# Kernel optimization log

Measured on AMD Instinct MI355X. Metric: run time of the kernel, lower is better.

## Reference

```python
import jax, jax.numpy as jnp
import numpy as np

N_ROW = 50000
N_COL = 50000
E = 1_200_000
D_IN = 64
D_H = 128


def _gconv(h_src, src, dst, w_e, W, b, n_src, n_dst):
    """DGL GraphConv(norm='both') with edge weights: symmetric degree norm
    (unweighted degrees, clamped to >=1), u_mul_e message, sum reduce, then linear."""
    ones = jnp.ones_like(w_e)
    out_deg = jnp.clip(jax.ops.segment_sum(ones, src, num_segments=n_src), 1.0)
    in_deg = jnp.clip(jax.ops.segment_sum(ones, dst, num_segments=n_dst), 1.0)
    hs = h_src * jax.lax.rsqrt(out_deg)[:, None]          # [n_src, F] pre-norm
    m = hs[src] * w_e[:, None]                            # [E, F] gather + edge weight
    agg = jax.ops.segment_sum(m, dst, num_segments=n_dst)  # [n_dst, F] scatter-sum
    agg = agg * jax.lax.rsqrt(in_deg)[:, None]
    return agg @ W + b


def setup_inputs() -> dict:
    key = jax.random.key(0)
    ks = jax.random.split(key, 16)
    return {
        'feat_row': jax.random.normal(ks[0], (N_ROW, D_IN), jnp.float32),
        'feat_col': jax.random.normal(ks[1], (N_COL, D_IN), jnp.float32),
        'src_rc': jax.random.randint(ks[2], (E,), 0, N_ROW),
        'dst_rc': jax.random.randint(ks[3], (E,), 0, N_COL),
        'w_rc': jax.random.uniform(ks[4], (E,), jnp.float32),
        'src_cr': jax.random.randint(ks[5], (E,), 0, N_COL),
        'dst_cr': jax.random.randint(ks[6], (E,), 0, N_ROW),
        'w_cr': jax.random.uniform(ks[7], (E,), jnp.float32),
        'W0_rc': jax.random.normal(ks[8], (D_IN, D_H), jnp.float32) / np.float32(np.sqrt(D_IN)),
        'b0_rc': jnp.zeros((D_H,), jnp.float32),
        'W0_cr': jax.random.normal(ks[9], (D_IN, D_H), jnp.float32) / np.float32(np.sqrt(D_IN)),
        'b0_cr': jnp.zeros((D_H,), jnp.float32),
        'W1_rc': jax.random.normal(ks[10], (D_H, D_H), jnp.float32) / np.float32(np.sqrt(D_H)),
        'b1_rc': jnp.zeros((D_H,), jnp.float32),
        'W1_cr': jax.random.normal(ks[11], (D_H, D_H), jnp.float32) / np.float32(np.sqrt(D_H)),
        'b1_cr': jnp.zeros((D_H,), jnp.float32),
    }


def reference(feat_row, feat_col, src_rc, dst_rc, w_rc, src_cr, dst_cr, w_cr,
              W0_rc, b0_rc, W0_cr, b0_cr, W1_rc, b1_rc, W1_cr, b1_cr):
    # Layer 1 (HeteroGraphConv, sum across relations; each dst type has one relation) + ReLU
    h_col1 = jax.nn.relu(_gconv(feat_row, src_rc, dst_rc, w_rc, W0_rc, b0_rc, N_ROW, N_COL))
    h_row1 = jax.nn.relu(_gconv(feat_col, src_cr, dst_cr, w_cr, W0_cr, b0_cr, N_COL, N_ROW))
    # Layer 2 + ReLU
    h_col2 = jax.nn.relu(_gconv(h_row1, src_rc, dst_rc, w_rc, W1_rc, b1_rc, N_ROW, N_COL))
    h_row2 = jax.nn.relu(_gconv(h_col1, src_cr, dst_cr, w_cr, W1_cr, b1_cr, N_COL, N_ROW))
    # dgl.mean_nodes per ntype (single graph -> [1, D_H]), summed over ntypes
    hg = jnp.mean(h_row2, axis=0, keepdims=True) + jnp.mean(h_col2, axis=0, keepdims=True)
    return hg
```

## Files before the change

kernel.cpp:

```cpp
#include <hip/hip_runtime.h>
#include <stdint.h>

constexpr int NROW = 50000;
constexpr int NCOL = 50000;
constexpr int DH   = 128;
constexpr int NTAB = 200000;
constexpr int HB   = 12500;
constexpr int HBLK = 64;
constexpr int DGRID = 1250;
constexpr int GGRID = 2048;
constexpr int CH    = 500;

typedef __attribute__((ext_vector_type(8))) short short8;
typedef __attribute__((ext_vector_type(4))) float f32x4;
typedef __attribute__((ext_vector_type(2))) float f32x2;

__device__ __forceinline__ float bf_hi(unsigned u) { return __uint_as_float(u & 0xffff0000u); }
__device__ __forceinline__ unsigned short f2bf(float f) {
    unsigned u = __float_as_uint(f);
    return (unsigned short)((u + 0x7fffu + ((u >> 16) & 1u)) >> 16);
}

__device__ __forceinline__ unsigned char f2fp8(float f) {
    unsigned b = __float_as_uint(f);
    unsigned s = (b >> 24) & 0x80u;
    unsigned mag = b & 0x7fffffffu;
    if (mag >= 0x43e00000u) return (unsigned char)(s | 0x7eu);
    unsigned r = mag + 0x7ffffu + ((mag >> 20) & 1u);
    int e = (int)(r >> 23) - 120;
    if (e < 1) {
        float af = __uint_as_float(mag);
        unsigned m = (unsigned)(af * 512.f + 0.5f);
        if (m > 8u) m = 8u;
        return (unsigned char)(s | m);
    }
    return (unsigned char)(s | (unsigned)(e << 3) | ((r >> 20) & 7u));
}

#if defined(__has_builtin) && __has_builtin(__builtin_amdgcn_cvt_pk_f32_fp8)
__device__ __forceinline__ f32x2 fp8x2f(unsigned v) {
    return __builtin_amdgcn_cvt_pk_f32_fp8((int)v, false);
}
__device__ __forceinline__ f32x4 fp8x4f(unsigned v) {
    f32x2 lo = __builtin_amdgcn_cvt_pk_f32_fp8((int)v, false);
    f32x2 hi = __builtin_amdgcn_cvt_pk_f32_fp8((int)v, true);
    f32x4 r; r.x = lo.x; r.y = lo.y; r.z = hi.x; r.w = hi.y; return r;
}
#else
__device__ __forceinline__ float fp8_1(unsigned u) {
    unsigned s = (u & 0x80u) << 24, em = u & 0x7fu;
    if (em >= 8u) return __uint_as_float(s | ((em + 960u) << 20));
    float v = (float)em * 0.001953125f;
    return (u & 0x80u) ? -v : v;
}
__device__ __forceinline__ f32x2 fp8x2f(unsigned v) {
    f32x2 r; r.x = fp8_1(v & 0xffu); r.y = fp8_1((v >> 8) & 0xffu); return r;
}
__device__ __forceinline__ f32x4 fp8x4f(unsigned v) {
    f32x4 r; r.x = fp8_1(v & 0xffu); r.y = fp8_1((v >> 8) & 0xffu);
    r.z = fp8_1((v >> 16) & 0xffu); r.w = fp8_1((v >> 24) & 0xffu); return r;
}
#endif

__global__ __launch_bounds__(512) void hist_lds(
        const int* __restrict__ s_rc, const int* __restrict__ d_rc,
        const int* __restrict__ s_cr, const int* __restrict__ d_cr,
        unsigned short* __restrict__ partial, int E) {
    __shared__ int h[HB];
    const int sec = blockIdx.x >> 6;
    const int blk = blockIdx.x & (HBLK - 1);
    const int tab = sec >> 2;
    const int lo  = (sec & 3) * HB;
    const int* __restrict__ arr = (tab == 0) ? s_rc : (tab == 1) ? d_rc
                                 : (tab == 2) ? s_cr : d_cr;
    for (int i = threadIdx.x; i < HB; i += blockDim.x) h[i] = 0;
    __syncthreads();
    const int stride = HBLK * blockDim.x;
    for (int i = blk * blockDim.x + threadIdx.x; i < E; i += stride) {
        int id = arr[i] - lo;
        if ((unsigned)id < (unsigned)HB) atomicAdd(&h[id], 1);
    }
    __syncthreads();
    unsigned short* __restrict__ out = partial + ((size_t)sec * HBLK + blk) * HB;
    for (int i = threadIdx.x; i < HB; i += blockDim.x) out[i] = (unsigned short)h[i];
}

__global__ void reduce_norms2(const unsigned short* __restrict__ partial, int* __restrict__ cnt,
                              float* __restrict__ norms) {
    int stride = gridDim.x * blockDim.x;
    for (int i = blockIdx.x * blockDim.x + threadIdx.x; i < NTAB; i += stride) {
        int t = i / 50000;
        int r = i - t * 50000;
        int q = r / HB;
        int j = r - q * HB;
        const unsigned short* __restrict__ p = partial + ((size_t)(t * 4 + q) * HBLK) * HB + j;
        int s = 0;
#pragma unroll
        for (int b = 0; b < HBLK; ++b) s += p[(size_t)b * HB];
        cnt[i] = s;
        norms[i] = 1.0f / sqrtf((float)max(s, 1));
    }
}

__global__ __launch_bounds__(256) void scanA(const int* __restrict__ cnt, int* __restrict__ bsum) {
    __shared__ int red[256];
    const int c = blockIdx.x;
    const int* __restrict__ cbl = cnt + ((c >= 100) ? 150000 : 50000);
    const int j0 = (c % 100) * CH;
    int s = 0;
    for (int i = threadIdx.x; i < CH; i += 256) s += cbl[j0 + i];
    red[threadIdx.x] = s;
    __syncthreads();
    for (int off = 128; off > 0; off >>= 1) {
        if (threadIdx.x < off) red[threadIdx.x] += red[threadIdx.x + off];
        __syncthreads();
    }
    if (threadIdx.x == 0) bsum[c] = red[0];
}

__global__ void scanB(const int* __restrict__ bsum, int* __restrict__ cbase) {
    __shared__ int b[200];
    for (int i = threadIdx.x; i < 200; i += blockDim.x) b[i] = bsum[i];
    __syncthreads();
    if (threadIdx.x < 2) {
        int run = 0;
        const int o = threadIdx.x * 100;
        for (int k = 0; k < 100; ++k) { cbase[o + k] = run; run += b[o + k]; }
    }
}

__global__ __launch_bounds__(512) void scanC(const int* __restrict__ cnt,
                                             const int* __restrict__ cbase,
                                             int* __restrict__ ptr_rc, int* __restrict__ ptr_cr,
                                             int E) {
    __shared__ int buf[512];
    const int c = blockIdx.x;
    const int table = (c >= 100);
    const int* __restrict__ cbl = cnt + (table ? 150000 : 50000);
    int* __restrict__ ptr = table ? ptr_cr : ptr_rc;
    const int j0 = (c % 100) * CH;
    const int t = threadIdx.x;
    const int v = (t < CH) ? cbl[j0 + t] : 0;
    buf[t] = v;
    __syncthreads();
    for (int off = 1; off < 512; off <<= 1) {
        int tmp = (t >= off) ? buf[t - off] : 0;
        __syncthreads();
        buf[t] += tmp;
        __syncthreads();
    }
    if (t < CH) ptr[j0 + t] = cbase[c] + buf[t] - v;
    if ((c % 100) == 99 && t == 0) ptr[50000] = E;
}

__global__ void block_starts(const unsigned short* __restrict__ partial, int* __restrict__ bstart,
                             const int* __restrict__ ptr_rc, const int* __restrict__ ptr_cr) {
    int stride = gridDim.x * blockDim.x;
    for (int i = blockIdx.x * blockDim.x + threadIdx.x; i < 8 * HB; i += stride) {
        int fsec = i / HB;
        int j = i - fsec * HB;
        int rel = fsec >> 2, q = fsec & 3;
        int histsec = rel * 8 + 4 + q;
        const int* __restrict__ ptr = rel ? ptr_cr : ptr_rc;
        int run = ptr[q * HB + j];
        const unsigned short* __restrict__ p = partial + ((size_t)histsec * HBLK) * HB + j;
        int* __restrict__ o = bstart + ((size_t)fsec * HBLK) * HB + j;
#pragma unroll
        for (int b = 0; b < HBLK; ++b) {
            o[(size_t)b * HB] = run;
            run += p[(size_t)b * HB];
        }
    }
}

__global__ __launch_bounds__(512) void csr_fill_sorted(
        const int* __restrict__ sA, const int* __restrict__ dA,
        const float* __restrict__ wA, const float* __restrict__ routA, unsigned* __restrict__ pairA,
        const int* __restrict__ sB, const int* __restrict__ dB,
        const float* __restrict__ wB, const float* __restrict__ routB, unsigned* __restrict__ pairB,
        const int* __restrict__ bstart, int E) {
    __shared__ int offs[HB];
    const int fsec = blockIdx.x & 7;
    const int blk  = blockIdx.x >> 3;
    const int rel = fsec >> 2, q = fsec & 3;
    const int lo = q * HB;
    const int* __restrict__ src  = rel ? sB : sA;
    const int* __restrict__ dst  = rel ? dB : dA;
    const float* __restrict__ w  = rel ? wB : wA;
    const float* __restrict__ ro = rel ? routB : routA;
    unsigned* __restrict__ pair  = rel ? pairB : pairA;
    const int* __restrict__ bs = bstart + ((size_t)fsec * HBLK + blk) * HB;
    for (int i = threadIdx.x; i < HB; i += blockDim.x) offs[i] = bs[i];
    __syncthreads();
    const int stride = HBLK * blockDim.x;
    for (int i = blk * blockDim.x + threadIdx.x; i < E; i += stride) {
        int id = dst[i] - lo;
        if ((unsigned)id < (unsigned)HB) {
            int pos = atomicAdd(&offs[id], 1);
            int s = src[i];
            pair[pos] = (unsigned)s | ((unsigned)f2bf(w[i] * ro[s]) << 16);
        }
    }
}

__global__ void prep_tables(const float4* __restrict__ fr, const float4* __restrict__ fc,
                            unsigned* __restrict__ f8r, unsigned* __restrict__ f8c, int nq,
                            const float* __restrict__ W0a, const float* __restrict__ W0b,
                            const float* __restrict__ W1a, const float* __restrict__ W1b,
                            unsigned short* __restrict__ wt) {
    const int total = 2 * nq + 49152;
    int stride = gridDim.x * blockDim.x;
    for (int i = blockIdx.x * blockDim.x + threadIdx.x; i < total; i += stride) {
        if (i < 2 * nq) {
            bool second = i >= nq;
            int k = second ? i - nq : i;
            float4 v = second ? fc[k] : fr[k];
            unsigned o = (unsigned)f2fp8(v.x) | ((unsigned)f2fp8(v.y) << 8)
                       | ((unsigned)f2fp8(v.z) << 16) | ((unsigned)f2fp8(v.w) << 24);
            if (second) f8c[k] = o; else f8r[k] = o;
        } else {
            int j = i - 2 * nq;
            const float* W; int K, base;
            if (j < 8192)       { W = W0a; K = 64;  base = 0; }
            else if (j < 16384) { W = W0b; K = 64;  base = 8192;  j -= 8192; }
            else if (j < 32768) { W = W1a; K = 128; base = 16384; j -= 16384; }
            else                { W = W1b; K = 128; base = 32768; j -= 32768; }
            int n = j / K, k = j - n * K;
            wt[base + n * K + k] = f2bf(W[k * DH + n]);
        }
    }
}

__global__ void gather64_2(const uint8_t* __restrict__ hA, const int* __restrict__ ptrA,
                           const unsigned* __restrict__ pairA, unsigned short* __restrict__ aggA,
                           const uint8_t* __restrict__ hB, const int* __restrict__ ptrB,
                           const unsigned* __restrict__ pairB, unsigned short* __restrict__ aggB,
                           int n) {
    const int low  = blockIdx.x & 7;
    const int rel  = low >> 2;
    const int bid  = (blockIdx.x >> 3) * 4 + (low & 3);
    const uint8_t* __restrict__ h = rel ? hB : hA;
    const int* __restrict__ ptr  = rel ? ptrB : ptrA;
    const unsigned* __restrict__ pair = rel ? pairB : pairA;
    unsigned short* __restrict__ agg  = rel ? aggB : aggA;
    const int gw   = (bid * blockDim.x + threadIdx.x) >> 6;
    const int nw   = (GGRID * blockDim.x) >> 6;
    const int lane = threadIdx.x & 63;
    const int qtr  = lane >> 4;
    const unsigned coff = (unsigned)((lane & 15) << 2);
    for (int node = gw; node < n; node += nw) {
        const int beg = ptr[node], end = ptr[node + 1];
        float a0[2] = {0.f, 0.f}, a1[2] = {0.f, 0.f}, a2[2] = {0.f, 0.f}, a3[2] = {0.f, 0.f};
        int j = beg + qtr;
        for (; j + 4 < end; j += 8) {
            unsigned p0 = pair[j], p1 = pair[j + 4];
            unsigned hv0 = *reinterpret_cast<const unsigned*>(&h[((p0 & 0xffffu) << 6) + coff]);
            unsigned hv1 = *reinterpret_cast<const unsigned*>(&h[((p1 & 0xffffu) << 6) + coff]);
            f32x4 d0 = fp8x4f(hv0), d1 = fp8x4f(hv1);
            float w0 = bf_hi(p0), w1 = bf_hi(p1);
            a0[0] = fmaf(d0.x, w0, a0[0]); a1[0] = fmaf(d0.y, w0, a1[0]);
            a2[0] = fmaf(d0.z, w0, a2[0]); a3[0] = fmaf(d0.w, w0, a3[0]);
            a0[1] = fmaf(d1.x, w1, a0[1]); a1[1] = fmaf(d1.y, w1, a1[1]);
            a2[1] = fmaf(d1.z, w1, a2[1]); a3[1] = fmaf(d1.w, w1, a3[1]);
        }
        for (; j < end; j += 4) {
            unsigned p = pair[j];
            unsigned hv = *reinterpret_cast<const unsigned*>(&h[((p & 0xffffu) << 6) + coff]);
            f32x4 d = fp8x4f(hv);
            float w = bf_hi(p);
            a0[0] = fmaf(d.x, w, a0[0]); a1[0] = fmaf(d.y, w, a1[0]);
            a2[0] = fmaf(d.z, w, a2[0]); a3[0] = fmaf(d.w, w, a3[0]);
        }
        float s0 = a0[0] + a0[1], s1 = a1[0] + a1[1];
        float s2 = a2[0] + a2[1], s3 = a3[0] + a3[1];
        s0 += __shfl_xor(s0, 16); s0 += __shfl_xor(s0, 32);
        s1 += __shfl_xor(s1, 16); s1 += __shfl_xor(s1, 32);
        s2 += __shfl_xor(s2, 16); s2 += __shfl_xor(s2, 32);
        s3 += __shfl_xor(s3, 16); s3 += __shfl_xor(s3, 32);
        if (lane < 16) {
            uint2 pk;
            pk.x = (unsigned)f2bf(s0) | ((unsigned)f2bf(s1) << 16);
            pk.y = (unsigned)f2bf(s2) | ((unsigned)f2bf(s3) << 16);
            *reinterpret_cast<uint2*>(&agg[(size_t)node * 64 + ((lane & 15) << 2)]) = pk;
        }
    }
}

__global__ __launch_bounds__(256) void dense64_2(
        const unsigned short* __restrict__ aggA, const float* __restrict__ rinA,
        const unsigned short* __restrict__ wtA, const float* __restrict__ bA,
        unsigned short* __restrict__ outA,
        const unsigned short* __restrict__ aggB, const float* __restrict__ rinB,
        const unsigned short* __restrict__ wtB, const float* __restrict__ bB,
        unsigned short* __restrict__ outB, int n) {
    constexpr int K = 64, NCH = 2;
    const int rel = blockIdx.x >= DGRID;
    const int bid = rel ? blockIdx.x - DGRID : blockIdx.x;
    const unsigned short* __restrict__ agg = rel ? aggB : aggA;
    const float* __restrict__ rin = rel ? rinB : rinA;
    const unsigned short* __restrict__ wt = rel ? wtB : wtA;
    const float* __restrict__ b = rel ? bB : bA;
    unsigned short* __restrict__ outbf = rel ? outB : outA;

    const int wave = threadIdx.x >> 6;
    const int lane = threadIdx.x & 63;
    const int lrow = lane & 15;
    const int kgrp = lane >> 4;
    const int c0   = wave * 32;

    short8 bfr[2][NCH];
#pragma unroll
    for (int t = 0; t < 2; ++t)
#pragma unroll
        for (int ch = 0; ch < NCH; ++ch)
            bfr[t][ch] = *reinterpret_cast<const short8*>(
                &wt[(size_t)(c0 + t * 16 + lrow) * K + ch * 32 + kgrp * 8]);

    const float bias0 = b[c0 + lrow], bias1 = b[c0 + 16 + lrow];
    const int nstrip = n >> 4;
    for (int s = bid; s < nstrip; s += DGRID) {
        const int r0 = s << 4;
        f32x4 d0 = {0.f, 0.f, 0.f, 0.f}, d1 = {0.f, 0.f, 0.f, 0.f};
#pragma unroll
        for (int ch = 0; ch < NCH; ++ch) {
            short8 af = *reinterpret_cast<const short8*>(
                &agg[(size_t)(r0 + lrow) * K + ch * 32 + kgrp * 8]);
            d0 = __builtin_amdgcn_mfma_f32_16x16x32_bf16(af, bfr[0][ch], d0, 0, 0, 0);
            d1 = __builtin_amdgcn_mfma_f32_16x16x32_bf16(af, bfr[1][ch], d1, 0, 0, 0);
        }
#pragma unroll
        for (int i = 0; i < 4; ++i) {
            const int row = r0 + kgrp * 4 + i;
            const float rv = rin[row];
            outbf[(size_t)row * DH + c0 + lrow]      = f2bf(fmaxf(fmaf(rv, d0[i], bias0), 0.f));
            outbf[(size_t)row * DH + c0 + 16 + lrow] = f2bf(fmaxf(fmaf(rv, d1[i], bias1), 0.f));
        }
    }
}

__global__ __launch_bounds__(256) void h1t_gemm2(
        const unsigned short* __restrict__ hA, const unsigned short* __restrict__ wtA,
        uint8_t* __restrict__ htA,
        const unsigned short* __restrict__ hB, const unsigned short* __restrict__ wtB,
        uint8_t* __restrict__ htB, int n) {
    constexpr int K = 128, NCH = 4;
    const int rel = blockIdx.x >= DGRID;
    const int bid = rel ? blockIdx.x - DGRID : blockIdx.x;
    const unsigned short* __restrict__ h = rel ? hB : hA;
    const unsigned short* __restrict__ wt = rel ? wtB : wtA;
    uint8_t* __restrict__ ht = rel ? htB : htA;

    const int wave = threadIdx.x >> 6;
    const int lane = threadIdx.x & 63;
    const int lrow = lane & 15;
    const int kgrp = lane >> 4;
    const int c0   = wave * 32;

    short8 bfr[2][NCH];
#pragma unroll
    for (int t = 0; t < 2; ++t)
#pragma unroll
        for (int ch = 0; ch < NCH; ++ch)
            bfr[t][ch] = *reinterpret_cast<const short8*>(
                &wt[(size_t)(c0 + t * 16 + lrow) * K + ch * 32 + kgrp * 8]);

    const int nstrip = n >> 4;
    for (int s = bid; s < nstrip; s += DGRID) {
        const int r0 = s << 4;
        f32x4 d0 = {0.f, 0.f, 0.f, 0.f}, d1 = {0.f, 0.f, 0.f, 0.f};
#pragma unroll
        for (int ch = 0; ch < NCH; ++ch) {
            short8 af = *reinterpret_cast<const short8*>(
                &h[(size_t)(r0 + lrow) * K + ch * 32 + kgrp * 8]);
            d0 = __builtin_amdgcn_mfma_f32_16x16x32_bf16(af, bfr[0][ch], d0, 0, 0, 0);
            d1 = __builtin_amdgcn_mfma_f32_16x16x32_bf16(af, bfr[1][ch], d1, 0, 0, 0);
        }
#pragma unroll
        for (int i = 0; i < 4; ++i) {
            const int row = r0 + kgrp * 4 + i;
            ht[(size_t)row * DH + c0 + lrow]      = f2fp8(d0[i]);
            ht[(size_t)row * DH + c0 + 16 + lrow] = f2fp8(d1[i]);
        }
    }
}

__global__ __launch_bounds__(256) void gather_final(
        const uint8_t* __restrict__ htA, const int* __restrict__ ptrA,
        const unsigned* __restrict__ pairA, const float* __restrict__ rinA,
        const float* __restrict__ bA,
        const uint8_t* __restrict__ htB, const int* __restrict__ ptrB,
        const unsigned* __restrict__ pairB, const float* __restrict__ rinB,
        const float* __restrict__ bB,
        float* __restrict__ partsum, int n, float invn) {
    const int low  = blockIdx.x & 7;
    const int rel  = low >> 2;
    const int chf  = (low >> 1) & 1;
    const int bid  = (blockIdx.x >> 3) * 2 + (low & 1);
    const uint8_t* __restrict__ ht = rel ? htB : htA;
    const int* __restrict__ ptr  = rel ? ptrB : ptrA;
    const unsigned* __restrict__ pair = rel ? pairB : pairA;
    const float* __restrict__ rin = rel ? rinB : rinA;
    const float* __restrict__ b   = rel ? bB : bA;

    const int gw   = (bid * blockDim.x + threadIdx.x) >> 6;
    const int nw   = ((GGRID / 2) * blockDim.x) >> 6;
    const int lane = threadIdx.x & 63;
    const int h2   = lane >> 5;
    const unsigned coff = (unsigned)(chf * 64 + ((lane & 31) << 1));
    const float b0v = b[coff], b1v = b[coff + 1];
    float m0 = 0.f, m1 = 0.f;

    for (int node = gw; node < n; node += nw) {
        const int beg = ptr[node], end = ptr[node + 1];
        float a0[4] = {0.f, 0.f, 0.f, 0.f}, a1[4] = {0.f, 0.f, 0.f, 0.f};
        int j = beg + h2;
        for (; j + 6 < end; j += 8) {
            unsigned p[4], hv[4];
#pragma unroll
            for (int u = 0; u < 4; ++u) p[u] = pair[j + 2 * u];
#pragma unroll
            for (int u = 0; u < 4; ++u)
                hv[u] = *reinterpret_cast<const unsigned short*>(&ht[((p[u] & 0xffffu) << 7) + coff]);
#pragma unroll
            for (int u = 0; u < 4; ++u) {
                f32x2 d = fp8x2f(hv[u]);
                float w = bf_hi(p[u]);
                a0[u] = fmaf(d.x, w, a0[u]);
                a1[u] = fmaf(d.y, w, a1[u]);
            }
        }
        for (; j < end; j += 2) {
            unsigned p = pair[j];
            unsigned hv = *reinterpret_cast<const unsigned short*>(&ht[((p & 0xffffu) << 7) + coff]);
            f32x2 d = fp8x2f(hv);
            float w = bf_hi(p);
            a0[0] = fmaf(d.x, w, a0[0]);
            a1[0] = fmaf(d.y, w, a1[0]);
        }
        float sx = (a0[0] + a0[1]) + (a0[2] + a0[3]);
        float sy = (a1[0] + a1[1]) + (a1[2] + a1[3]);
        sx += __shfl_xor(sx, 32);
        sy += __shfl_xor(sy, 32);
        const float rv = rin[node];
        m0 += fmaxf(fmaf(rv, sx, b0v), 0.f);
        m1 += fmaxf(fmaf(rv, sy, b1v), 0.f);
    }

    __shared__ float red[4][64];
    const int wv = threadIdx.x >> 6;
    if (h2 == 0) {
        red[wv][(lane & 31) * 2]     = m0;
        red[wv][(lane & 31) * 2 + 1] = m1;
    }
    __syncthreads();
    if (threadIdx.x < 64) {
        float s = red[0][threadIdx.x] + red[1][threadIdx.x]
                + red[2][threadIdx.x] + red[3][threadIdx.x];
        partsum[(size_t)blockIdx.x * 64 + threadIdx.x] = s * invn;
    }
}

__global__ void reduce_out2(const float* __restrict__ partsum, float* __restrict__ out, int nblk) {
    const int t = threadIdx.x;
    const int ch = t >> 6, c = t & 63;
    float s = 0.f;
    for (int b = blockIdx.x; b < nblk; b += gridDim.x)
        if (((b >> 1) & 1) == ch) s += partsum[(size_t)b * 64 + c];
    atomicAdd(&out[t], s);
}

extern "C" void kernel_launch(void* const* d_in, const int* in_sizes, int n_in,
                              void* d_out, int out_size, void* d_ws, size_t ws_size,
                              hipStream_t stream) {
    const float* feat_row = (const float*)d_in[0];
    const float* feat_col = (const float*)d_in[1];
    const int*   src_rc   = (const int*)d_in[2];
    const int*   dst_rc   = (const int*)d_in[3];
    const float* w_rc     = (const float*)d_in[4];
    const int*   src_cr   = (const int*)d_in[5];
    const int*   dst_cr   = (const int*)d_in[6];
    const float* w_cr     = (const float*)d_in[7];
    const float* W0_rc    = (const float*)d_in[8];
    const float* b0_rc    = (const float*)d_in[9];
    const float* W0_cr    = (const float*)d_in[10];
    const float* b0_cr    = (const float*)d_in[11];
    const float* W1_rc    = (const float*)d_in[12];
    const float* b1_rc    = (const float*)d_in[13];
    const float* W1_cr    = (const float*)d_in[14];
    const float* b1_cr    = (const float*)d_in[15];
    const int E = in_sizes[2];
    float* out = (float*)d_out;

    int*   cnt     = (int*)d_ws;
    float* norms   = (float*)(cnt + 200000);
    int*   ptr_rc  = (int*)(norms + 200000);
    int*   ptr_cr  = ptr_rc + 50004;
    int*   bsum    = ptr_cr + 50004;
    int*   cbase   = bsum + 200;
    unsigned* pair_rc = (unsigned*)(cbase + 216);
    unsigned* pair_cr = pair_rc + E;
    unsigned short* agg_col = (unsigned short*)(pair_cr + E);
    unsigned short* agg_row = agg_col + (size_t)NCOL * 64;
    uint8_t* f8_row = (uint8_t*)(agg_row + (size_t)NROW * 64);
    uint8_t* f8_col = f8_row + (size_t)NROW * 64;
    unsigned short* h_col1 = (unsigned short*)(f8_col + (size_t)NCOL * 64);
    unsigned short* h_row1 = h_col1 + (size_t)NCOL * DH;
    uint8_t* ht_row = (uint8_t*)(h_row1 + (size_t)NROW * DH);
    uint8_t* ht_col = ht_row + (size_t)NROW * DH;
    float* partsum = (float*)(ht_col + (size_t)NCOL * DH);
    unsigned short* wt = (unsigned short*)(partsum + (size_t)2 * GGRID * DH);
    unsigned short* partial = (unsigned short*)agg_col;
    int* bstart = (int*)(partial + (size_t)16 * HBLK * HB);

    float* r_out_rc = norms;
    float* r_in_rc  = norms + NROW;
    float* r_out_cr = norms + NROW + NCOL;
    float* r_in_cr  = norms + NROW + 2 * NCOL;

    unsigned short* wt0_rc = wt;
    unsigned short* wt0_cr = wt + 8192;
    unsigned short* wt1_rc = wt + 16384;
    unsigned short* wt1_cr = wt + 32768;

    hist_lds<<<16 * HBLK, 512, 0, stream>>>(src_rc, dst_rc, src_cr, dst_cr, partial, E);
    reduce_norms2<<<512, 256, 0, stream>>>(partial, cnt, norms);
    scanA<<<200, 256, 0, stream>>>(cnt, bsum);
    scanB<<<1, 256, 0, stream>>>(bsum, cbase);
    scanC<<<200, 512, 0, stream>>>(cnt, cbase, ptr_rc, ptr_cr, E);
    block_starts<<<400, 256, 0, stream>>>(partial, bstart, ptr_rc, ptr_cr);
    csr_fill_sorted<<<8 * HBLK, 512, 0, stream>>>(
        src_rc, dst_rc, w_rc, r_out_rc, pair_rc,
        src_cr, dst_cr, w_cr, r_out_cr, pair_cr, bstart, E);

    prep_tables<<<2048, 256, 0, stream>>>((const float4*)feat_row, (const float4*)feat_col,
                                          (unsigned*)f8_row, (unsigned*)f8_col, NROW * 64 / 4,
                                          W0_rc, W0_cr, W1_rc, W1_cr, wt);

    gather64_2<<<2 * GGRID, 256, 0, stream>>>(f8_row, ptr_rc, pair_rc, agg_col,
                                              f8_col, ptr_cr, pair_cr, agg_row, NCOL);
    dense64_2<<<2 * DGRID, 256, 0, stream>>>(agg_col, r_in_rc, wt0_rc, b0_rc, h_col1,
                                             agg_row, r_in_cr, wt0_cr, b0_cr, h_row1, NCOL);

    h1t_gemm2<<<2 * DGRID, 256, 0, stream>>>(h_row1, wt1_rc, ht_row,
                                             h_col1, wt1_cr, ht_col, NROW);
    hipMemsetAsync(out, 0, DH * sizeof(float), stream);
    gather_final<<<2 * GGRID, 256, 0, stream>>>(
        ht_row, ptr_rc, pair_rc, r_in_rc, b1_rc,
        ht_col, ptr_cr, pair_cr, r_in_cr, b1_cr,
        partsum, NCOL, 1.0f / NCOL);
    reduce_out2<<<64, 128, 0, stream>>>(partsum, out, 2 * GGRID);
}
```

Baseline: 347.0 us.

## Split fp8 layer-2 table into two 64-column halves and widen gather64 unroll

The fp8 output of the layer-2 transform is stored as two separate 64-byte-per-row tables, one per column half, instead of a single 128-byte-row table. Each gather_final pass then touches a compact table with a denser row stride, which is meant to improve cache locality. Separately, gather64_2 now uses half-waves with 2 columns per lane and 8 independent edge loads in flight instead of quarter-waves with 4 columns. This raises memory-level parallelism at the cost of narrower per-lane loads and more registers.

```diff
diff --git a/kernel.cpp b/kernel.cpp
--- a/kernel.cpp
+++ b/kernel.cpp
@@ -41,11 +41,6 @@
 __device__ __forceinline__ f32x2 fp8x2f(unsigned v) {
     return __builtin_amdgcn_cvt_pk_f32_fp8((int)v, false);
 }
-__device__ __forceinline__ f32x4 fp8x4f(unsigned v) {
-    f32x2 lo = __builtin_amdgcn_cvt_pk_f32_fp8((int)v, false);
-    f32x2 hi = __builtin_amdgcn_cvt_pk_f32_fp8((int)v, true);
-    f32x4 r; r.x = lo.x; r.y = lo.y; r.z = hi.x; r.w = hi.y; return r;
-}
 #else
 __device__ __forceinline__ float fp8_1(unsigned u) {
     unsigned s = (u & 0x80u) << 24, em = u & 0x7fu;
@@ -55,10 +50,6 @@
 }
 __device__ __forceinline__ f32x2 fp8x2f(unsigned v) {
     f32x2 r; r.x = fp8_1(v & 0xffu); r.y = fp8_1((v >> 8) & 0xffu); return r;
-}
-__device__ __forceinline__ f32x4 fp8x4f(unsigned v) {
-    f32x4 r; r.x = fp8_1(v & 0xffu); r.y = fp8_1((v >> 8) & 0xffu);
-    r.z = fp8_1((v >> 16) & 0xffu); r.w = fp8_1((v >> 24) & 0xffu); return r;
 }
 #endif
 
@@ -246,42 +237,42 @@
     const int gw   = (bid * blockDim.x + threadIdx.x) >> 6;
     const int nw   = (GGRID * blockDim.x) >> 6;
     const int lane = threadIdx.x & 63;
-    const int qtr  = lane >> 4;
-    const unsigned coff = (unsigned)((lane & 15) << 2);
+    const int half = lane >> 5;
+    const int c    = (lane & 31) << 1;
     for (int node = gw; node < n; node += nw) {
         const int beg = ptr[node], end = ptr[node + 1];
-        float a0[2] = {0.f, 0.f}, a1[2] = {0.f, 0.f}, a2[2] = {0.f, 0.f}, a3[2] = {0.f, 0.f};
-        int j = beg + qtr;
-        for (; j + 4 < end; j += 8) {
-            unsigned p0 = pair[j], p1 = pair[j + 4];
-            unsigned hv0 = *reinterpret_cast<const unsigned*>(&h[((p0 & 0xffffu) << 6) + coff]);
-            unsigned hv1 = *reinterpret_cast<const unsigned*>(&h[((p1 & 0xffffu) << 6) + coff]);
-            f32x4 d0 = fp8x4f(hv0), d1 = fp8x4f(hv1);
-            float w0 = bf_hi(p0), w1 = bf_hi(p1);
-            a0[0] = fmaf(d0.x, w0, a0[0]); a1[0] = fmaf(d0.y, w0, a1[0]);
-            a2[0] = fmaf(d0.z, w0, a2[0]); a3[0] = fmaf(d0.w, w0, a3[0]);
-            a0[1] = fmaf(d1.x, w1, a0[1]); a1[1] = fmaf(d1.y, w1, a1[1]);
-            a2[1] = fmaf(d1.z, w1, a2[1]); a3[1] = fmaf(d1.w, w1, a3[1]);
-        }
-        for (; j < end; j += 4) {
+        float ax[8], ay[8];
+#pragma unroll
+        for (int u = 0; u < 8; ++u) { ax[u] = 0.f; ay[u] = 0.f; }
+        int j = beg + half;
+        for (; j + 14 < end; j += 16) {
+            unsigned p[8], hv[8];
+#pragma unroll
+            for (int u = 0; u < 8; ++u) p[u] = pair[j + 2 * u];
+#pragma unroll
+            for (int u = 0; u < 8; ++u)
+                hv[u] = *reinterpret_cast<const unsigned short*>(&h[((p[u] & 0xffffu) << 6) + c]);
+#pragma unroll
+            for (int u = 0; u < 8; ++u) {
+                f32x2 d = fp8x2f(hv[u]);
+                float w = bf_hi(p[u]);
+                ax[u] = fmaf(d.x, w, ax[u]); ay[u] = fmaf(d.y, w, ay[u]);
+            }
+        }
+        for (; j < end; j += 2) {
             unsigned p = pair[j];
-            unsigned hv = *reinterpret_cast<const unsigned*>(&h[((p & 0xffffu) << 6) + coff]);
-            f32x4 d = fp8x4f(hv);
+            unsigned hv = *reinterpret_cast<const unsigned short*>(&h[((p & 0xffffu) << 6) + c]);
+            f32x2 d = fp8x2f(hv);
             float w = bf_hi(p);
-            a0[0] = fmaf(d.x, w, a0[0]); a1[0] = fmaf(d.y, w, a1[0]);
-            a2[0] = fmaf(d.z, w, a2[0]); a3[0] = fmaf(d.w, w, a3[0]);
-        }
-        float s0 = a0[0] + a0[1], s1 = a1[0] + a1[1];
-        float s2 = a2[0] + a2[1], s3 = a3[0] + a3[1];
-        s0 += __shfl_xor(s0, 16); s0 += __shfl_xor(s0, 32);
-        s1 += __shfl_xor(s1, 16); s1 += __shfl_xor(s1, 32);
-        s2 += __shfl_xor(s2, 16); s2 += __shfl_xor(s2, 32);
-        s3 += __shfl_xor(s3, 16); s3 += __shfl_xor(s3, 32);
-        if (lane < 16) {
-            uint2 pk;
-            pk.x = (unsigned)f2bf(s0) | ((unsigned)f2bf(s1) << 16);
-            pk.y = (unsigned)f2bf(s2) | ((unsigned)f2bf(s3) << 16);
-            *reinterpret_cast<uint2*>(&agg[(size_t)node * 64 + ((lane & 15) << 2)]) = pk;
+            ax[0] = fmaf(d.x, w, ax[0]); ay[0] = fmaf(d.y, w, ay[0]);
+        }
+        float ax_ = ((ax[0] + ax[1]) + (ax[2] + ax[3])) + ((ax[4] + ax[5]) + (ax[6] + ax[7]));
+        float ay_ = ((ay[0] + ay[1]) + (ay[2] + ay[3])) + ((ay[4] + ay[5]) + (ay[6] + ay[7]));
+        ax_ += __shfl_xor(ax_, 32);
+        ay_ += __shfl_xor(ay_, 32);
+        if (half == 0) {
+            unsigned pk = (unsigned)f2bf(ax_) | ((unsigned)f2bf(ay_) << 16);
+            *reinterpret_cast<unsigned*>(&agg[(size_t)node * 64 + c]) = pk;
         }
     }
 }
@@ -340,21 +331,22 @@
 
 __global__ __launch_bounds__(256) void h1t_gemm2(
         const unsigned short* __restrict__ hA, const unsigned short* __restrict__ wtA,
-        uint8_t* __restrict__ htA,
+        uint8_t* __restrict__ htA0, uint8_t* __restrict__ htA1,
         const unsigned short* __restrict__ hB, const unsigned short* __restrict__ wtB,
-        uint8_t* __restrict__ htB, int n) {
+        uint8_t* __restrict__ htB0, uint8_t* __restrict__ htB1, int n) {
     constexpr int K = 128, NCH = 4;
     const int rel = blockIdx.x >= DGRID;
     const int bid = rel ? blockIdx.x - DGRID : blockIdx.x;
     const unsigned short* __restrict__ h = rel ? hB : hA;
     const unsigned short* __restrict__ wt = rel ? wtB : wtA;
-    uint8_t* __restrict__ ht = rel ? htB : htA;
 
     const int wave = threadIdx.x >> 6;
     const int lane = threadIdx.x & 63;
     const int lrow = lane & 15;
     const int kgrp = lane >> 4;
     const int c0   = wave * 32;
+    uint8_t* __restrict__ ht = (wave < 2) ? (rel ? htB0 : htA0) : (rel ? htB1 : htA1);
+    const int cb = c0 & 63;
 
     short8 bfr[2][NCH];
 #pragma unroll
@@ -378,25 +370,25 @@
 #pragma unroll
         for (int i = 0; i < 4; ++i) {
             const int row = r0 + kgrp * 4 + i;
-            ht[(size_t)row * DH + c0 + lrow]      = f2fp8(d0[i]);
-            ht[(size_t)row * DH + c0 + 16 + lrow] = f2fp8(d1[i]);
+            ht[((size_t)row << 6) + cb + lrow]      = f2fp8(d0[i]);
+            ht[((size_t)row << 6) + cb + 16 + lrow] = f2fp8(d1[i]);
         }
     }
 }
 
 __global__ __launch_bounds__(256) void gather_final(
-        const uint8_t* __restrict__ htA, const int* __restrict__ ptrA,
-        const unsigned* __restrict__ pairA, const float* __restrict__ rinA,
-        const float* __restrict__ bA,
-        const uint8_t* __restrict__ htB, const int* __restrict__ ptrB,
-        const unsigned* __restrict__ pairB, const float* __restrict__ rinB,
-        const float* __restrict__ bB,
+        const uint8_t* __restrict__ htA0, const uint8_t* __restrict__ htA1,
+        const int* __restrict__ ptrA, const unsigned* __restrict__ pairA,
+        const float* __restrict__ rinA, const float* __restrict__ bA,
+        const uint8_t* __restrict__ htB0, const uint8_t* __restrict__ htB1,
+        const int* __restrict__ ptrB, const unsigned* __restrict__ pairB,
+        const float* __restrict__ rinB, const float* __restrict__ bB,
         float* __restrict__ partsum, int n, float invn) {
     const int low  = blockIdx.x & 7;
     const int rel  = low >> 2;
     const int chf  = (low >> 1) & 1;
     const int bid  = (blockIdx.x >> 3) * 2 + (low & 1);
-    const uint8_t* __restrict__ ht = rel ? htB : htA;
+    const uint8_t* __restrict__ ht = rel ? (chf ? htB1 : htB0) : (chf ? htA1 : htA0);
     const int* __restrict__ ptr  = rel ? ptrB : ptrA;
     const unsigned* __restrict__ pair = rel ? pairB : pairA;
     const float* __restrict__ rin = rel ? rinB : rinA;
@@ -406,8 +398,8 @@
     const int nw   = ((GGRID / 2) * blockDim.x) >> 6;
     const int lane = threadIdx.x & 63;
     const int h2   = lane >> 5;
-    const unsigned coff = (unsigned)(chf * 64 + ((lane & 31) << 1));
-    const float b0v = b[coff], b1v = b[coff + 1];
+    const unsigned coff = (unsigned)((lane & 31) << 1);
+    const float b0v = b[chf * 64 + coff], b1v = b[chf * 64 + coff + 1];
     float m0 = 0.f, m1 = 0.f;
 
     for (int node = gw; node < n; node += nw) {
@@ -420,7 +412,7 @@
             for (int u = 0; u < 4; ++u) p[u] = pair[j + 2 * u];
 #pragma unroll
             for (int u = 0; u < 4; ++u)
-                hv[u] = *reinterpret_cast<const unsigned short*>(&ht[((p[u] & 0xffffu) << 7) + coff]);
+                hv[u] = *reinterpret_cast<const unsigned short*>(&ht[((p[u] & 0xffffu) << 6) + coff]);
 #pragma unroll
             for (int u = 0; u < 4; ++u) {
                 f32x2 d = fp8x2f(hv[u]);
@@ -431,7 +423,7 @@
         }
         for (; j < end; j += 2) {
             unsigned p = pair[j];
-            unsigned hv = *reinterpret_cast<const unsigned short*>(&ht[((p & 0xffffu) << 7) + coff]);
+            unsigned hv = *reinterpret_cast<const unsigned short*>(&ht[((p & 0xffffu) << 6) + coff]);
             f32x2 d = fp8x2f(hv);
             float w = bf_hi(p);
             a0[0] = fmaf(d.x, w, a0[0]);
@@ -505,10 +497,12 @@
     uint8_t* f8_col = f8_row + (size_t)NROW * 64;
     unsigned short* h_col1 = (unsigned short*)(f8_col + (size_t)NCOL * 64);
     unsigned short* h_row1 = h_col1 + (size_t)NCOL * DH;
-    uint8_t* ht_row = (uint8_t*)(h_row1 + (size_t)NROW * DH);
-    uint8_t* ht_col = ht_row + (size_t)NROW * DH;
-    float* partsum = (float*)(ht_col + (size_t)NCOL * DH);
-    unsigned short* wt = (unsigned short*)(partsum + (size_t)2 * GGRID * DH);
+    uint8_t* ht_row0 = (uint8_t*)(h_row1 + (size_t)NROW * DH);
+    uint8_t* ht_row1 = ht_row0 + (size_t)NROW * 64;
+    uint8_t* ht_col0 = ht_row1 + (size_t)NROW * 64;
+    uint8_t* ht_col1 = ht_col0 + (size_t)NCOL * 64;
+    float* partsum = (float*)(ht_col1 + (size_t)NCOL * 64);
+    unsigned short* wt = (unsigned short*)(partsum + (size_t)2 * GGRID * 64);
     unsigned short* partial = (unsigned short*)agg_col;
     int* bstart = (int*)(partial + (size_t)16 * HBLK * HB);
 
@@ -541,12 +535,12 @@
     dense64_2<<<2 * DGRID, 256, 0, stream>>>(agg_col, r_in_rc, wt0_rc, b0_rc, h_col1,
                                              agg_row, r_in_cr, wt0_cr, b0_cr, h_row1, NCOL);
 
-    h1t_gemm2<<<2 * DGRID, 256, 0, stream>>>(h_row1, wt1_rc, ht_row,
-                                             h_col1, wt1_cr, ht_col, NROW);
+    h1t_gemm2<<<2 * DGRID, 256, 0, stream>>>(h_row1, wt1_rc, ht_row0, ht_row1,
+                                             h_col1, wt1_cr, ht_col0, ht_col1, NROW);
     hipMemsetAsync(out, 0, DH * sizeof(float), stream);
     gather_final<<<2 * GGRID, 256, 0, stream>>>(
-        ht_row, ptr_rc, pair_rc, r_in_rc, b1_rc,
-        ht_col, ptr_cr, pair_cr, r_in_cr, b1_cr,
+        ht_row0, ht_row1, ptr_rc, pair_rc, r_in_rc, b1_rc,
+        ht_col0, ht_col1, ptr_cr, pair_cr, r_in_cr, b1_cr,
         partsum, NCOL, 1.0f / NCOL);
     reduce_out2<<<64, 128, 0, stream>>>(partsum, out, 2 * GGRID);
 }
```

Result: faster. 336.2 us (-3.1%).
